# Performance work log

Hardware: AMD Instinct MI355X
Metric: run time of the kernel (lower is better)

The kernel has to match this reference:

```python
import jax, jax.numpy as jnp
import numpy as np

EPS_LN = 1e-5

def layer_norm(x, g, b):
    mu = x.mean(-1, keepdims=True)
    var = ((x - mu) ** 2).mean(-1, keepdims=True)
    return (x - mu) / jnp.sqrt(var + EPS_LN) * g + b

def spike(x):
    # MultiSpike: quantized spike activation, forward = clip(round(x), 0, 4)
    return jnp.clip(jnp.round(x), 0.0, 4.0)

def setup_inputs() -> dict:
    key = jax.random.key(0)
    ks = jax.random.split(key, 8)
    B, C, H, W = 16, 256, 56, 56
    hid = 128
    inp = {}
    inp['feature_map'] = jax.random.normal(ks[0], (B, C, H, W), jnp.float32)
    inp['audio_feature'] = jax.random.normal(ks[1], (B, 1, C), jnp.float32)
    # MINE params
    inp['w1'] = jax.random.normal(ks[2], (hid, 2 * C), jnp.float32) / np.sqrt(2 * C)
    inp['b1'] = jnp.zeros((hid,), jnp.float32)
    inp['g1'] = jnp.ones((hid,), jnp.float32)
    inp['beta1'] = jnp.zeros((hid,), jnp.float32)
    inp['w2'] = jax.random.normal(ks[3], (hid // 2, hid), jnp.float32) / np.sqrt(hid)
    inp['b2'] = jnp.zeros((hid // 2,), jnp.float32)
    inp['g2'] = jnp.ones((hid // 2,), jnp.float32)
    inp['beta2'] = jnp.zeros((hid // 2,), jnp.float32)
    inp['w3'] = jax.random.normal(ks[4], (1, hid // 2), jnp.float32) / np.sqrt(hid // 2)
    inp['b3'] = jnp.zeros((1,), jnp.float32)
    # MI params
    inp['pw'] = jax.random.normal(ks[5], (C, C), jnp.float32) / np.sqrt(C)
    inp['pb'] = jnp.zeros((C,), jnp.float32)
    inp['pg'] = jnp.ones((C,), jnp.float32)
    inp['pbeta'] = jnp.zeros((C,), jnp.float32)
    return inp

def reference(feature_map, audio_feature, w1, b1, g1, beta1, w2, b2, g2, beta2,
              w3, b3, pw, pb, pg, pbeta):
    B, C, H, W = feature_map.shape
    # visual tokens: [B*H*W, C]
    visual = feature_map.transpose(0, 2, 3, 1).reshape(B * H * W, C)
    # broadcast audio to every spatial position: [B*H*W, C]
    audio = jnp.broadcast_to(audio_feature[:, 0][:, None, None, :], (B, H, W, C)).reshape(B * H * W, C)
    # MINE MLP on joint features
    joint = jnp.concatenate([visual, audio], axis=1)            # [BHW, 2C]
    h = spike(layer_norm(joint @ w1.T + b1, g1, beta1))          # [BHW, 128]
    h = spike(layer_norm(h @ w2.T + b2, g2, beta2))              # [BHW, 64]
    mi = (h @ w3.T + b3)[:, 0]                                   # [BHW]
    mi_map = mi.reshape(B, 1, H * W)
    fm_flat = feature_map.reshape(B, C, H * W)
    # MI-weighted pooling: [B,1,C]
    x = jnp.einsum('bos,bcs->boc', mi_map, fm_flat)
    x = x @ pw.T + pb                                            # proj (dropout = eval identity)
    x = spike(layer_norm(x, pg, pbeta))                          # [B,1,C]
    fusion_map = jnp.einsum('bchw,bc->bchw', feature_map, x[:, 0])
    mi4 = mi_map.reshape(B, 1, H, W)
    mi4 = (mi4 - mi4.min()) / (mi4.max() - mi4.min() + 1e-6)     # global min-max norm
    return fusion_map, mi4
```

## Files before the change

kernel.cpp:

```cpp
#include <hip/hip_runtime.h>

#define HW 3136
#define NPOS 12845056
#define KC 32

__device__ __forceinline__ unsigned fkey(float f) {
  unsigned u = __float_as_uint(f);
  return (u & 0x80000000u) ? ~u : (u | 0x80000000u);
}
__device__ __forceinline__ float funkey(unsigned u) {
  return __uint_as_float((u & 0x80000000u) ? (u & 0x7FFFFFFFu) : ~u);
}
__device__ __forceinline__ float spikef(float x) {
  return fminf(fmaxf(rintf(x), 0.0f), 4.0f);
}

__global__ __launch_bounds__(256) void prep_kernel(
    const float* __restrict__ audio, const float* __restrict__ w1,
    const float* __restrict__ b1, const float* __restrict__ w2,
    float* __restrict__ a_pre, float* __restrict__ w1t,
    float* __restrict__ w2t, float* __restrict__ pool,
    unsigned* __restrict__ mm)
{
  __shared__ float au[256];
  const int bx = blockIdx.x, t = threadIdx.x;
  if (bx < 128) {
    int idx = bx * 256 + t;
    int c = idx >> 7, j = idx & 127;
    w1t[idx] = w1[j * 512 + c];
  } else if (bx < 160) {
    int idx = (bx - 128) * 256 + t;
    int k = idx >> 6, j2 = idx & 63;
    w2t[idx] = w2[j2 * 128 + k];
  } else if (bx < 176) {
    int b = bx - 160;
    au[t] = audio[b * 256 + t];
    __syncthreads();
    int w = t >> 6, l = t & 63;
    float a0 = au[l], a1 = au[l + 64], a2 = au[l + 128], a3 = au[l + 192];
    for (int jj = 0; jj < 32; ++jj) {
      int j = w * 32 + jj;
      const float* row = w1 + j * 512 + 256;
      float s = row[l] * a0 + row[l + 64] * a1 + row[l + 128] * a2 + row[l + 192] * a3;
      #pragma unroll
      for (int off = 32; off; off >>= 1) s += __shfl_xor(s, off);
      if (l == 0) a_pre[b * 128 + j] = s + b1[j];
    }
  } else {
    for (int i = t; i < 4096; i += 256) pool[i] = 0.0f;
    if (t == 0) { mm[0] = 0xFFFFFFFFu; mm[1] = 0u; }
  }
}

__global__ __launch_bounds__(256, 3) void mlp_kernel(
    const float* __restrict__ fm, const float* __restrict__ w1t,
    const float* __restrict__ w2t, const float* __restrict__ b2,
    const float* __restrict__ w3, const float* __restrict__ b3,
    const float* __restrict__ g1, const float* __restrict__ be1,
    const float* __restrict__ g2, const float* __restrict__ be2,
    const float* __restrict__ a_pre, float* __restrict__ mi_out,
    float* __restrict__ pool, unsigned* __restrict__ mm)
{
  __shared__ __align__(16) unsigned char smem[49152];
  __shared__ float red1[16][64];
  __shared__ float miL[64];

  float* fmb = (float*)smem;
  float* wb1 = (float*)(smem + 16384);
  float* h1f = (float*)smem;
  float* w2b = (float*)(smem + 32768);

  const int b  = blockIdx.y;
  const int s0 = blockIdx.x * 64;
  const int t  = threadIdx.x;
  const int l  = t & 63;
  const int w  = t >> 6;
  const int pg = t & 15;
  const int jg = t >> 4;

  const float* fmblk = fm + (size_t)b * 256 * HW + s0;

  auto stage1 = [&](int ch, int bd) {
    const int r0 = w * 8;
    #pragma unroll
    for (int q = 0; q < 2; ++q) {
      int row = r0 + q * 4 + (l >> 4);
      const float* g = fmblk + (size_t)(ch * KC + row) * HW + (l & 15) * 4;
      float* d = fmb + (bd * KC + r0 + q * 4) * 64;
      __builtin_amdgcn_global_load_lds(
          (const __attribute__((address_space(1))) void*)g,
          (__attribute__((address_space(3))) void*)d, 16, 0, 0);
    }
    #pragma unroll
    for (int q = 0; q < 4; ++q) {
      int row = r0 + q * 2 + (l >> 5);
      const float* g = w1t + (size_t)(ch * KC + row) * 128 + (l & 31) * 4;
      float* d = wb1 + (bd * KC + r0 + q * 2) * 128;
      __builtin_amdgcn_global_load_lds(
          (const __attribute__((address_space(1))) void*)g,
          (__attribute__((address_space(3))) void*)d, 16, 0, 0);
    }
  };
  auto stage2 = [&](int kc, int bd) {
    const int r0 = w * 8;
    #pragma unroll
    for (int q = 0; q < 2; ++q) {
      int row = r0 + q * 4 + (l >> 4);
      const float* g = w2t + (size_t)(kc * KC + row) * 64 + (l & 15) * 4;
      float* d = w2b + (bd * KC + r0 + q * 4) * 64;
      __builtin_amdgcn_global_load_lds(
          (const __attribute__((address_space(1))) void*)g,
          (__attribute__((address_space(3))) void*)d, 16, 0, 0);
    }
  };

  float acc[4][8];
  #pragma unroll
  for (int pp = 0; pp < 4; ++pp)
    #pragma unroll
    for (int jj = 0; jj < 8; ++jj) acc[pp][jj] = 0.f;

  stage1(0, 0);
  #pragma unroll 1
  for (int ch = 0; ch < 8; ++ch) {
    __syncthreads();
    if (ch < 7) stage1(ch + 1, (ch + 1) & 1);
    const float* fb = fmb + (ch & 1) * KC * 64;
    const float* wb = wb1 + (ch & 1) * KC * 128;
    #pragma unroll 4
    for (int k = 0; k < KC; ++k) {
      float4 xf = *(const float4*)(fb + k * 64 + pg * 4);
      float4 w0 = *(const float4*)(wb + k * 128 + jg * 8);
      float4 w1v = *(const float4*)(wb + k * 128 + jg * 8 + 4);
      float xs[4] = {xf.x, xf.y, xf.z, xf.w};
      float wv[8] = {w0.x, w0.y, w0.z, w0.w, w1v.x, w1v.y, w1v.z, w1v.w};
      #pragma unroll
      for (int pp = 0; pp < 4; ++pp)
        #pragma unroll
        for (int jj = 0; jj < 8; ++jj)
          acc[pp][jj] = fmaf(xs[pp], wv[jj], acc[pp][jj]);
    }
  }
  {
    float4 a0 = *(const float4*)(a_pre + b * 128 + jg * 8);
    float4 a1 = *(const float4*)(a_pre + b * 128 + jg * 8 + 4);
    float aw[8] = {a0.x, a0.y, a0.z, a0.w, a1.x, a1.y, a1.z, a1.w};
    #pragma unroll
    for (int pp = 0; pp < 4; ++pp)
      #pragma unroll
      for (int jj = 0; jj < 8; ++jj) acc[pp][jj] += aw[jj];
  }

  {
    float4 ps;
    float* p = &ps.x;
    #pragma unroll
    for (int pp = 0; pp < 4; ++pp) {
      float s = 0.f;
      #pragma unroll
      for (int jj = 0; jj < 8; ++jj) s += acc[pp][jj];
      p[pp] = s;
    }
    __syncthreads();
    *(float4*)&red1[jg][pg * 4] = ps;
  }
  __syncthreads();
  float mu[4];
  {
    float4 s = make_float4(0.f, 0.f, 0.f, 0.f);
    #pragma unroll
    for (int q = 0; q < 16; ++q) {
      float4 v = *(const float4*)&red1[q][pg * 4];
      s.x += v.x; s.y += v.y; s.z += v.z; s.w += v.w;
    }
    mu[0] = s.x * (1.0f/128.0f); mu[1] = s.y * (1.0f/128.0f);
    mu[2] = s.z * (1.0f/128.0f); mu[3] = s.w * (1.0f/128.0f);
  }
  __syncthreads();
  {
    float4 vs;
    float* p = &vs.x;
    #pragma unroll
    for (int pp = 0; pp < 4; ++pp) {
      float s = 0.f;
      #pragma unroll
      for (int jj = 0; jj < 8; ++jj) { float d = acc[pp][jj] - mu[pp]; s = fmaf(d, d, s); }
      p[pp] = s;
    }
    *(float4*)&red1[jg][pg * 4] = vs;
  }
  __syncthreads();
  float inv[4];
  {
    float4 s = make_float4(0.f, 0.f, 0.f, 0.f);
    #pragma unroll
    for (int q = 0; q < 16; ++q) {
      float4 v = *(const float4*)&red1[q][pg * 4];
      s.x += v.x; s.y += v.y; s.z += v.z; s.w += v.w;
    }
    inv[0] = 1.0f / sqrtf(s.x * (1.0f/128.0f) + 1e-5f);
    inv[1] = 1.0f / sqrtf(s.y * (1.0f/128.0f) + 1e-5f);
    inv[2] = 1.0f / sqrtf(s.z * (1.0f/128.0f) + 1e-5f);
    inv[3] = 1.0f / sqrtf(s.w * (1.0f/128.0f) + 1e-5f);
  }
  __syncthreads();

  stage2(0, 0);
  {
    float4 g1a = *(const float4*)(g1 + jg * 8);
    float4 g1b = *(const float4*)(g1 + jg * 8 + 4);
    float4 ba  = *(const float4*)(be1 + jg * 8);
    float4 bb  = *(const float4*)(be1 + jg * 8 + 4);
    float gv[8] = {g1a.x, g1a.y, g1a.z, g1a.w, g1b.x, g1b.y, g1b.z, g1b.w};
    float bv[8] = {ba.x, ba.y, ba.z, ba.w, bb.x, bb.y, bb.z, bb.w};
    #pragma unroll
    for (int jj = 0; jj < 8; ++jj) {
      float4 hv;
      hv.x = spikef((acc[0][jj] - mu[0]) * inv[0] * gv[jj] + bv[jj]);
      hv.y = spikef((acc[1][jj] - mu[1]) * inv[1] * gv[jj] + bv[jj]);
      hv.z = spikef((acc[2][jj] - mu[2]) * inv[2] * gv[jj] + bv[jj]);
      hv.w = spikef((acc[3][jj] - mu[3]) * inv[3] * gv[jj] + bv[jj]);
      *(float4*)(h1f + (jg * 8 + jj) * 64 + pg * 4) = hv;
    }
  }
  __syncthreads();

  float a2[4][4];
  #pragma unroll
  for (int pp = 0; pp < 4; ++pp)
    #pragma unroll
    for (int jj = 0; jj < 4; ++jj) a2[pp][jj] = 0.f;
  #pragma unroll 1
  for (int kc = 0; kc < 4; ++kc) {
    if (kc < 3) stage2(kc + 1, (kc + 1) & 1);
    const float* wb = w2b + (kc & 1) * KC * 64;
    #pragma unroll 4
    for (int k = 0; k < KC; ++k) {
      float4 hf = *(const float4*)(h1f + (kc * KC + k) * 64 + pg * 4);
      float4 wv4 = *(const float4*)(wb + k * 64 + jg * 4);
      float hs[4] = {hf.x, hf.y, hf.z, hf.w};
      float wv[4] = {wv4.x, wv4.y, wv4.z, wv4.w};
      #pragma unroll
      for (int pp = 0; pp < 4; ++pp)
        #pragma unroll
        for (int jj = 0; jj < 4; ++jj)
          a2[pp][jj] = fmaf(hs[pp], wv[jj], a2[pp][jj]);
    }
    __syncthreads();
  }

  float h2[4][4];
  {
    float4 b2v = *(const float4*)(b2 + jg * 4);
    float bb[4] = {b2v.x, b2v.y, b2v.z, b2v.w};
    float4 ps;
    float* p = &ps.x;
    #pragma unroll
    for (int pp = 0; pp < 4; ++pp) {
      float s = 0.f;
      #pragma unroll
      for (int jj = 0; jj < 4; ++jj) { h2[pp][jj] = a2[pp][jj] + bb[jj]; s += h2[pp][jj]; }
      p[pp] = s;
    }
    *(float4*)&red1[jg][pg * 4] = ps;
  }
  __syncthreads();
  float mu2[4];
  {
    float4 s = make_float4(0.f, 0.f, 0.f, 0.f);
    #pragma unroll
    for (int q = 0; q < 16; ++q) {
      float4 v = *(const float4*)&red1[q][pg * 4];
      s.x += v.x; s.y += v.y; s.z += v.z; s.w += v.w;
    }
    mu2[0] = s.x * (1.0f/64.0f); mu2[1] = s.y * (1.0f/64.0f);
    mu2[2] = s.z * (1.0f/64.0f); mu2[3] = s.w * (1.0f/64.0f);
  }
  __syncthreads();
  {
    float4 vs;
    float* p = &vs.x;
    #pragma unroll
    for (int pp = 0; pp < 4; ++pp) {
      float s = 0.f;
      #pragma unroll
      for (int jj = 0; jj < 4; ++jj) { float d = h2[pp][jj] - mu2[pp]; s = fmaf(d, d, s); }
      p[pp] = s;
    }
    *(float4*)&red1[jg][pg * 4] = vs;
  }
  __syncthreads();
  float inv2[4];
  {
    float4 s = make_float4(0.f, 0.f, 0.f, 0.f);
    #pragma unroll
    for (int q = 0; q < 16; ++q) {
      float4 v = *(const float4*)&red1[q][pg * 4];
      s.x += v.x; s.y += v.y; s.z += v.z; s.w += v.w;
    }
    inv2[0] = 1.0f / sqrtf(s.x * (1.0f/64.0f) + 1e-5f);
    inv2[1] = 1.0f / sqrtf(s.y * (1.0f/64.0f) + 1e-5f);
    inv2[2] = 1.0f / sqrtf(s.z * (1.0f/64.0f) + 1e-5f);
    inv2[3] = 1.0f / sqrtf(s.w * (1.0f/64.0f) + 1e-5f);
  }
  __syncthreads();
  {
    float4 g2v = *(const float4*)(g2 + jg * 4);
    float4 be2v = *(const float4*)(be2 + jg * 4);
    float4 w3v = *(const float4*)(w3 + jg * 4);
    float gv[4] = {g2v.x, g2v.y, g2v.z, g2v.w};
    float bv[4] = {be2v.x, be2v.y, be2v.z, be2v.w};
    float wv[4] = {w3v.x, w3v.y, w3v.z, w3v.w};
    float4 ps;
    float* p = &ps.x;
    #pragma unroll
    for (int pp = 0; pp < 4; ++pp) {
      float s = 0.f;
      #pragma unroll
      for (int jj = 0; jj < 4; ++jj) {
        float sp = spikef((h2[pp][jj] - mu2[pp]) * inv2[pp] * gv[jj] + bv[jj]);
        s = fmaf(sp, wv[jj], s);
      }
      p[pp] = s;
    }
    *(float4*)&red1[jg][pg * 4] = ps;
  }
  __syncthreads();
  if (t < 16) {
    float4 s = make_float4(0.f, 0.f, 0.f, 0.f);
    #pragma unroll
    for (int q = 0; q < 16; ++q) {
      float4 v = *(const float4*)&red1[q][pg * 4];
      s.x += v.x; s.y += v.y; s.z += v.z; s.w += v.w;
    }
    float b3v = b3[0];
    float4 miv = make_float4(s.x + b3v, s.y + b3v, s.z + b3v, s.w + b3v);
    *(float4*)(mi_out + b * HW + s0 + pg * 4) = miv;
    *(float4*)(miL + pg * 4) = miv;
    float mn = fminf(fminf(miv.x, miv.y), fminf(miv.z, miv.w));
    float mx = fmaxf(fmaxf(miv.x, miv.y), fmaxf(miv.z, miv.w));
    #pragma unroll
    for (int off = 8; off; off >>= 1) {
      mn = fminf(mn, __shfl_xor(mn, off));
      mx = fmaxf(mx, __shfl_xor(mx, off));
    }
    if (t == 0) {
      unsigned kmn = fkey(mn), kmx = fkey(mx);
      volatile unsigned* vmm = (volatile unsigned*)mm;
      if (kmn < vmm[0]) atomicMin(&mm[0], kmn);
      if (kmx > vmm[1]) atomicMax(&mm[1], kmx);
    }
  }
  __syncthreads();

  const float miv = miL[l];
  const float* fmp = fmblk + l;
  #pragma unroll 4
  for (int ci = 0; ci < 64; ++ci) {
    int c = (w << 6) + ci;
    float v = fmp[(size_t)c * HW] * miv;
    #pragma unroll
    for (int off = 32; off; off >>= 1) v += __shfl_xor(v, off);
    if (l == 0) atomicAdd(&pool[b * 256 + c], v);
  }
}

__global__ __launch_bounds__(256) void scale_kernel(
    const float* __restrict__ pool, const float* __restrict__ pw,
    const float* __restrict__ pb, const float* __restrict__ pg,
    const float* __restrict__ pbeta, float* __restrict__ scale,
    const unsigned* __restrict__ mm, float* __restrict__ gpar)
{
  __shared__ float pl[256];
  __shared__ float xsh[256];
  __shared__ float rs[4], rs2[4];
  int b = blockIdx.x, t = threadIdx.x;
  pl[t] = pool[b*256 + t];
  __syncthreads();
  int w = t >> 6, l = t & 63;
  float p0 = pl[l], p1 = pl[l+64], p2 = pl[l+128], p3 = pl[l+192];
  for (int jj = 0; jj < 64; ++jj) {
    int j = w*64 + jj;
    const float* row = pw + j*256;
    float s = row[l]*p0 + row[l+64]*p1 + row[l+128]*p2 + row[l+192]*p3;
    #pragma unroll
    for (int off = 32; off; off >>= 1) s += __shfl_xor(s, off);
    if (l == 0) xsh[j] = s;
  }
  __syncthreads();
  float x = xsh[t] + pb[t];
  float s = x;
  #pragma unroll
  for (int off = 32; off; off >>= 1) s += __shfl_xor(s, off);
  if (l == 0) rs[w] = s;
  __syncthreads();
  float mu = (rs[0]+rs[1]+rs[2]+rs[3]) * (1.0f/256.0f);
  float d = x - mu;
  float s2 = d*d;
  #pragma unroll
  for (int off = 32; off; off >>= 1) s2 += __shfl_xor(s2, off);
  if (l == 0) rs2[w] = s2;
  __syncthreads();
  float var = (rs2[0]+rs2[1]+rs2[2]+rs2[3]) * (1.0f/256.0f);
  float v = d / sqrtf(var + 1e-5f) * pg[t] + pbeta[t];
  scale[b*256 + t] = spikef(v);
  if (b == 0 && t == 0) {
    float mn = funkey(mm[0]), mx = funkey(mm[1]);
    gpar[0] = mn;
    gpar[1] = mx - mn + 1e-6f;
  }
}

__global__ __launch_bounds__(256) void fuse_kernel(
    const float4* __restrict__ fm4, const float* __restrict__ scale,
    const float4* __restrict__ mi4, const float* __restrict__ gpar,
    float4* __restrict__ out4, float4* __restrict__ mi4out)
{
  const int c = blockIdx.x, b = blockIdx.y, t = threadIdx.x;
  if (c < 256) {
    float s = scale[b * 256 + c];
    size_t base = ((size_t)b * 256 + c) * 784;
    #pragma unroll
    for (int i = 0; i < 3; ++i) {
      int idx = t + i * 256;
      float4 v = fm4[base + idx];
      out4[base + idx] = make_float4(v.x*s, v.y*s, v.z*s, v.w*s);
    }
    int idx = t + 768;
    if (idx < 784) {
      float4 v = fm4[base + idx];
      out4[base + idx] = make_float4(v.x*s, v.y*s, v.z*s, v.w*s);
    }
  } else {
    float gmin = gpar[0], den = gpar[1];
    size_t base = (size_t)b * 784;
    #pragma unroll
    for (int i = 0; i < 3; ++i) {
      int idx = t + i * 256;
      float4 v = mi4[base + idx];
      mi4out[base + idx] = make_float4((v.x-gmin)/den, (v.y-gmin)/den,
                                       (v.z-gmin)/den, (v.w-gmin)/den);
    }
    int idx = t + 768;
    if (idx < 784) {
      float4 v = mi4[base + idx];
      mi4out[base + idx] = make_float4((v.x-gmin)/den, (v.y-gmin)/den,
                                       (v.z-gmin)/den, (v.w-gmin)/den);
    }
  }
}

extern "C" void kernel_launch(void* const* d_in, const int* in_sizes, int n_in,
                              void* d_out, int out_size, void* d_ws, size_t ws_size,
                              hipStream_t stream)
{
  const float* fm    = (const float*)d_in[0];
  const float* audio = (const float*)d_in[1];
  const float* w1    = (const float*)d_in[2];
  const float* b1    = (const float*)d_in[3];
  const float* g1    = (const float*)d_in[4];
  const float* be1   = (const float*)d_in[5];
  const float* w2    = (const float*)d_in[6];
  const float* b2    = (const float*)d_in[7];
  const float* g2    = (const float*)d_in[8];
  const float* be2   = (const float*)d_in[9];
  const float* w3    = (const float*)d_in[10];
  const float* b3    = (const float*)d_in[11];
  const float* pw    = (const float*)d_in[12];
  const float* pb    = (const float*)d_in[13];
  const float* pg    = (const float*)d_in[14];
  const float* pbeta = (const float*)d_in[15];

  float* ws    = (float*)d_ws;
  float* a_pre = ws;
  float* pool  = ws + 2048;
  float* scale = ws + 6144;
  float* mi    = ws + 10240;
  float* w1t   = ws + 60416;
  float* w2t   = ws + 93184;
  unsigned* mm = (unsigned*)(ws + 101376);
  float* gpar  = ws + 101378;

  float* out    = (float*)d_out;
  float* mi4out = out + NPOS;

  prep_kernel<<<177, 256, 0, stream>>>(audio, w1, b1, w2, a_pre, w1t, w2t,
                                       pool, mm);
  mlp_kernel<<<dim3(49, 16), 256, 0, stream>>>(fm, w1t, w2t, b2, w3, b3,
                                               g1, be1, g2, be2,
                                               a_pre, mi, pool, mm);
  scale_kernel<<<16, 256, 0, stream>>>(pool, pw, pb, pg, pbeta, scale, mm, gpar);
  fuse_kernel<<<dim3(257, 16), 256, 0, stream>>>((const float4*)fm, scale,
                                                 (const float4*)mi, gpar,
                                                 (float4*)out, (float4*)mi4out);
}
```

Before: 308.3 us.

## Restructure MLP kernel to one position per lane with wave-uniform weight reads

Replaces the LDS-staged, double-buffered register-tiled GEMM in the MLP kernel with a mapping where each lane owns one spatial position and each wave owns a slice of output features. Weights are read directly from global memory at wave-uniform addresses, so they can be served as scalar or broadcast loads, and activations are read straight from the feature map. LayerNorm reductions become a simple 4-wave sum through a small shared array. This removes the LDS staging traffic and many barriers, but gives up the 4x8 register reuse of x across features and relies on cached global weight reads.

Result: faster. 287.0 us (-6.9%).

```diff
diff --git a/kernel.cpp b/kernel.cpp
--- a/kernel.cpp
+++ b/kernel.cpp
@@ -2,7 +2,6 @@
 
 #define HW 3136
 #define NPOS 12845056
-#define KC 32
 
 __device__ __forceinline__ unsigned fkey(float f) {
   unsigned u = __float_as_uint(f);
@@ -61,307 +60,162 @@
     const float* __restrict__ a_pre, float* __restrict__ mi_out,
     float* __restrict__ pool, unsigned* __restrict__ mm)
 {
-  __shared__ __align__(16) unsigned char smem[49152];
-  __shared__ float red1[16][64];
-  __shared__ float miL[64];
-
-  float* fmb = (float*)smem;
-  float* wb1 = (float*)(smem + 16384);
-  float* h1f = (float*)smem;
-  float* w2b = (float*)(smem + 32768);
+  __shared__ float h1f[128 * 64];
+  __shared__ float red[8][64];
 
   const int b  = blockIdx.y;
   const int s0 = blockIdx.x * 64;
   const int t  = threadIdx.x;
   const int l  = t & 63;
-  const int w  = t >> 6;
-  const int pg = t & 15;
-  const int jg = t >> 4;
+  const int wv = __builtin_amdgcn_readfirstlane(t >> 6);
 
   const float* fmblk = fm + (size_t)b * 256 * HW + s0;
 
-  auto stage1 = [&](int ch, int bd) {
-    const int r0 = w * 8;
-    #pragma unroll
-    for (int q = 0; q < 2; ++q) {
-      int row = r0 + q * 4 + (l >> 4);
-      const float* g = fmblk + (size_t)(ch * KC + row) * HW + (l & 15) * 4;
-      float* d = fmb + (bd * KC + r0 + q * 4) * 64;
-      __builtin_amdgcn_global_load_lds(
-          (const __attribute__((address_space(1))) void*)g,
-          (__attribute__((address_space(3))) void*)d, 16, 0, 0);
-    }
+  float acc[32];
+  #pragma unroll
+  for (int j = 0; j < 32; ++j) acc[j] = 0.f;
+  {
+    const float*  fp = fmblk + l;
+    const float4* wr = (const float4*)(w1t + wv * 32);
+    #pragma unroll 4
+    for (int k = 0; k < 256; ++k) {
+      float x = *fp; fp += HW;
+      #pragma unroll
+      for (int q = 0; q < 8; ++q) {
+        float4 w4 = wr[q];
+        acc[4*q+0] = fmaf(x, w4.x, acc[4*q+0]);
+        acc[4*q+1] = fmaf(x, w4.y, acc[4*q+1]);
+        acc[4*q+2] = fmaf(x, w4.z, acc[4*q+2]);
+        acc[4*q+3] = fmaf(x, w4.w, acc[4*q+3]);
+      }
+      wr += 32;
+    }
+  }
+  {
+    const float4* ap = (const float4*)(a_pre + b * 128 + wv * 32);
+    #pragma unroll
+    for (int q = 0; q < 8; ++q) {
+      float4 a4 = ap[q];
+      acc[4*q+0] += a4.x; acc[4*q+1] += a4.y;
+      acc[4*q+2] += a4.z; acc[4*q+3] += a4.w;
+    }
+  }
+
+  float mu, inv;
+  {
+    float s = 0.f;
+    #pragma unroll
+    for (int j = 0; j < 32; ++j) s += acc[j];
+    red[wv][l] = s;
+    __syncthreads();
+    mu = (red[0][l] + red[1][l] + red[2][l] + red[3][l]) * (1.0f/128.0f);
+    float s2 = 0.f;
+    #pragma unroll
+    for (int j = 0; j < 32; ++j) { float d = acc[j] - mu; s2 = fmaf(d, d, s2); }
+    red[4 + wv][l] = s2;
+    __syncthreads();
+    float var = (red[4][l] + red[5][l] + red[6][l] + red[7][l]) * (1.0f/128.0f);
+    inv = 1.0f / sqrtf(var + 1e-5f);
+  }
+
+  {
+    const float* gp = g1  + wv * 32;
+    const float* bp = be1 + wv * 32;
+    #pragma unroll
+    for (int j = 0; j < 32; ++j) {
+      float h = spikef((acc[j] - mu) * inv * gp[j] + bp[j]);
+      h1f[(wv * 32 + j) * 64 + l] = h;
+    }
+  }
+  __syncthreads();
+
+  float a2[16];
+  #pragma unroll
+  for (int j = 0; j < 16; ++j) a2[j] = 0.f;
+  {
+    const float*  hp = h1f + l;
+    const float4* wr = (const float4*)(w2t + wv * 16);
+    #pragma unroll 4
+    for (int k = 0; k < 128; ++k) {
+      float h = *hp; hp += 64;
+      #pragma unroll
+      for (int q = 0; q < 4; ++q) {
+        float4 w4 = wr[q];
+        a2[4*q+0] = fmaf(h, w4.x, a2[4*q+0]);
+        a2[4*q+1] = fmaf(h, w4.y, a2[4*q+1]);
+        a2[4*q+2] = fmaf(h, w4.z, a2[4*q+2]);
+        a2[4*q+3] = fmaf(h, w4.w, a2[4*q+3]);
+      }
+      wr += 16;
+    }
+  }
+  {
+    const float4* bp = (const float4*)(b2 + wv * 16);
     #pragma unroll
     for (int q = 0; q < 4; ++q) {
-      int row = r0 + q * 2 + (l >> 5);
-      const float* g = w1t + (size_t)(ch * KC + row) * 128 + (l & 31) * 4;
-      float* d = wb1 + (bd * KC + r0 + q * 2) * 128;
-      __builtin_amdgcn_global_load_lds(
-          (const __attribute__((address_space(1))) void*)g,
-          (__attribute__((address_space(3))) void*)d, 16, 0, 0);
-    }
-  };
-  auto stage2 = [&](int kc, int bd) {
-    const int r0 = w * 8;
-    #pragma unroll
-    for (int q = 0; q < 2; ++q) {
-      int row = r0 + q * 4 + (l >> 4);
-      const float* g = w2t + (size_t)(kc * KC + row) * 64 + (l & 15) * 4;
-      float* d = w2b + (bd * KC + r0 + q * 4) * 64;
-      __builtin_amdgcn_global_load_lds(
-          (const __attribute__((address_space(1))) void*)g,
-          (__attribute__((address_space(3))) void*)d, 16, 0, 0);
-    }
-  };
-
-  float acc[4][8];
-  #pragma unroll
-  for (int pp = 0; pp < 4; ++pp)
-    #pragma unroll
-    for (int jj = 0; jj < 8; ++jj) acc[pp][jj] = 0.f;
-
-  stage1(0, 0);
-  #pragma unroll 1
-  for (int ch = 0; ch < 8; ++ch) {
-    __syncthreads();
-    if (ch < 7) stage1(ch + 1, (ch + 1) & 1);
-    const float* fb = fmb + (ch & 1) * KC * 64;
-    const float* wb = wb1 + (ch & 1) * KC * 128;
-    #pragma unroll 4
-    for (int k = 0; k < KC; ++k) {
-      float4 xf = *(const float4*)(fb + k * 64 + pg * 4);
-      float4 w0 = *(const float4*)(wb + k * 128 + jg * 8);
-      float4 w1v = *(const float4*)(wb + k * 128 + jg * 8 + 4);
-      float xs[4] = {xf.x, xf.y, xf.z, xf.w};
-      float wv[8] = {w0.x, w0.y, w0.z, w0.w, w1v.x, w1v.y, w1v.z, w1v.w};
-      #pragma unroll
-      for (int pp = 0; pp < 4; ++pp)
-        #pragma unroll
-        for (int jj = 0; jj < 8; ++jj)
-          acc[pp][jj] = fmaf(xs[pp], wv[jj], acc[pp][jj]);
-    }
-  }
-  {
-    float4 a0 = *(const float4*)(a_pre + b * 128 + jg * 8);
-    float4 a1 = *(const float4*)(a_pre + b * 128 + jg * 8 + 4);
-    float aw[8] = {a0.x, a0.y, a0.z, a0.w, a1.x, a1.y, a1.z, a1.w};
-    #pragma unroll
-    for (int pp = 0; pp < 4; ++pp)
-      #pragma unroll
-      for (int jj = 0; jj < 8; ++jj) acc[pp][jj] += aw[jj];
-  }
-
-  {
-    float4 ps;
-    float* p = &ps.x;
-    #pragma unroll
-    for (int pp = 0; pp < 4; ++pp) {
-      float s = 0.f;
-      #pragma unroll
-      for (int jj = 0; jj < 8; ++jj) s += acc[pp][jj];
-      p[pp] = s;
-    }
-    __syncthreads();
-    *(float4*)&red1[jg][pg * 4] = ps;
-  }
-  __syncthreads();
-  float mu[4];
-  {
-    float4 s = make_float4(0.f, 0.f, 0.f, 0.f);
-    #pragma unroll
-    for (int q = 0; q < 16; ++q) {
-      float4 v = *(const float4*)&red1[q][pg * 4];
-      s.x += v.x; s.y += v.y; s.z += v.z; s.w += v.w;
-    }
-    mu[0] = s.x * (1.0f/128.0f); mu[1] = s.y * (1.0f/128.0f);
-    mu[2] = s.z * (1.0f/128.0f); mu[3] = s.w * (1.0f/128.0f);
-  }
-  __syncthreads();
-  {
-    float4 vs;
-    float* p = &vs.x;
-    #pragma unroll
-    for (int pp = 0; pp < 4; ++pp) {
-      float s = 0.f;
-      #pragma unroll
-      for (int jj = 0; jj < 8; ++jj) { float d = acc[pp][jj] - mu[pp]; s = fmaf(d, d, s); }
-      p[pp] = s;
-    }
-    *(float4*)&red1[jg][pg * 4] = vs;
-  }
-  __syncthreads();
-  float inv[4];
-  {
-    float4 s = make_float4(0.f, 0.f, 0.f, 0.f);
-    #pragma unroll
-    for (int q = 0; q < 16; ++q) {
-      float4 v = *(const float4*)&red1[q][pg * 4];
-      s.x += v.x; s.y += v.y; s.z += v.z; s.w += v.w;
-    }
-    inv[0] = 1.0f / sqrtf(s.x * (1.0f/128.0f) + 1e-5f);
-    inv[1] = 1.0f / sqrtf(s.y * (1.0f/128.0f) + 1e-5f);
-    inv[2] = 1.0f / sqrtf(s.z * (1.0f/128.0f) + 1e-5f);
-    inv[3] = 1.0f / sqrtf(s.w * (1.0f/128.0f) + 1e-5f);
-  }
-  __syncthreads();
-
-  stage2(0, 0);
-  {
-    float4 g1a = *(const float4*)(g1 + jg * 8);
-    float4 g1b = *(const float4*)(g1 + jg * 8 + 4);
-    float4 ba  = *(const float4*)(be1 + jg * 8);
-    float4 bb  = *(const float4*)(be1 + jg * 8 + 4);
-    float gv[8] = {g1a.x, g1a.y, g1a.z, g1a.w, g1b.x, g1b.y, g1b.z, g1b.w};
-    float bv[8] = {ba.x, ba.y, ba.z, ba.w, bb.x, bb.y, bb.z, bb.w};
-    #pragma unroll
-    for (int jj = 0; jj < 8; ++jj) {
-      float4 hv;
-      hv.x = spikef((acc[0][jj] - mu[0]) * inv[0] * gv[jj] + bv[jj]);
-      hv.y = spikef((acc[1][jj] - mu[1]) * inv[1] * gv[jj] + bv[jj]);
-      hv.z = spikef((acc[2][jj] - mu[2]) * inv[2] * gv[jj] + bv[jj]);
-      hv.w = spikef((acc[3][jj] - mu[3]) * inv[3] * gv[jj] + bv[jj]);
-      *(float4*)(h1f + (jg * 8 + jj) * 64 + pg * 4) = hv;
-    }
-  }
-  __syncthreads();
-
-  float a2[4][4];
-  #pragma unroll
-  for (int pp = 0; pp < 4; ++pp)
-    #pragma unroll
-    for (int jj = 0; jj < 4; ++jj) a2[pp][jj] = 0.f;
-  #pragma unroll 1
-  for (int kc = 0; kc < 4; ++kc) {
-    if (kc < 3) stage2(kc + 1, (kc + 1) & 1);
-    const float* wb = w2b + (kc & 1) * KC * 64;
-    #pragma unroll 4
-    for (int k = 0; k < KC; ++k) {
-      float4 hf = *(const float4*)(h1f + (kc * KC + k) * 64 + pg * 4);
-      float4 wv4 = *(const float4*)(wb + k * 64 + jg * 4);
-      float hs[4] = {hf.x, hf.y, hf.z, hf.w};
-      float wv[4] = {wv4.x, wv4.y, wv4.z, wv4.w};
-      #pragma unroll
-      for (int pp = 0; pp < 4; ++pp)
-        #pragma unroll
-        for (int jj = 0; jj < 4; ++jj)
-          a2[pp][jj] = fmaf(hs[pp], wv[jj], a2[pp][jj]);
-    }
-    __syncthreads();
-  }
-
-  float h2[4][4];
-  {
-    float4 b2v = *(const float4*)(b2 + jg * 4);
-    float bb[4] = {b2v.x, b2v.y, b2v.z, b2v.w};
-    float4 ps;
-    float* p = &ps.x;
-    #pragma unroll
-    for (int pp = 0; pp < 4; ++pp) {
-      float s = 0.f;
-      #pragma unroll
-      for (int jj = 0; jj < 4; ++jj) { h2[pp][jj] = a2[pp][jj] + bb[jj]; s += h2[pp][jj]; }
-      p[pp] = s;
-    }
-    *(float4*)&red1[jg][pg * 4] = ps;
-  }
-  __syncthreads();
-  float mu2[4];
-  {
-    float4 s = make_float4(0.f, 0.f, 0.f, 0.f);
-    #pragma unroll
-    for (int q = 0; q < 16; ++q) {
-      float4 v = *(const float4*)&red1[q][pg * 4];
-      s.x += v.x; s.y += v.y; s.z += v.z; s.w += v.w;
-    }
-    mu2[0] = s.x * (1.0f/64.0f); mu2[1] = s.y * (1.0f/64.0f);
-    mu2[2] = s.z * (1.0f/64.0f); mu2[3] = s.w * (1.0f/64.0f);
-  }
-  __syncthreads();
-  {
-    float4 vs;
-    float* p = &vs.x;
-    #pragma unroll
-    for (int pp = 0; pp < 4; ++pp) {
-      float s = 0.f;
-      #pragma unroll
-      for (int jj = 0; jj < 4; ++jj) { float d = h2[pp][jj] - mu2[pp]; s = fmaf(d, d, s); }
-      p[pp] = s;
-    }
-    *(float4*)&red1[jg][pg * 4] = vs;
-  }
-  __syncthreads();
-  float inv2[4];
-  {
-    float4 s = make_float4(0.f, 0.f, 0.f, 0.f);
-    #pragma unroll
-    for (int q = 0; q < 16; ++q) {
-      float4 v = *(const float4*)&red1[q][pg * 4];
-      s.x += v.x; s.y += v.y; s.z += v.z; s.w += v.w;
-    }
-    inv2[0] = 1.0f / sqrtf(s.x * (1.0f/64.0f) + 1e-5f);
-    inv2[1] = 1.0f / sqrtf(s.y * (1.0f/64.0f) + 1e-5f);
-    inv2[2] = 1.0f / sqrtf(s.z * (1.0f/64.0f) + 1e-5f);
-    inv2[3] = 1.0f / sqrtf(s.w * (1.0f/64.0f) + 1e-5f);
-  }
-  __syncthreads();
-  {
-    float4 g2v = *(const float4*)(g2 + jg * 4);
-    float4 be2v = *(const float4*)(be2 + jg * 4);
-    float4 w3v = *(const float4*)(w3 + jg * 4);
-    float gv[4] = {g2v.x, g2v.y, g2v.z, g2v.w};
-    float bv[4] = {be2v.x, be2v.y, be2v.z, be2v.w};
-    float wv[4] = {w3v.x, w3v.y, w3v.z, w3v.w};
-    float4 ps;
-    float* p = &ps.x;
-    #pragma unroll
-    for (int pp = 0; pp < 4; ++pp) {
-      float s = 0.f;
-      #pragma unroll
-      for (int jj = 0; jj < 4; ++jj) {
-        float sp = spikef((h2[pp][jj] - mu2[pp]) * inv2[pp] * gv[jj] + bv[jj]);
-        s = fmaf(sp, wv[jj], s);
-      }
-      p[pp] = s;
-    }
-    *(float4*)&red1[jg][pg * 4] = ps;
-  }
-  __syncthreads();
-  if (t < 16) {
-    float4 s = make_float4(0.f, 0.f, 0.f, 0.f);
-    #pragma unroll
-    for (int q = 0; q < 16; ++q) {
-      float4 v = *(const float4*)&red1[q][pg * 4];
-      s.x += v.x; s.y += v.y; s.z += v.z; s.w += v.w;
-    }
-    float b3v = b3[0];
-    float4 miv = make_float4(s.x + b3v, s.y + b3v, s.z + b3v, s.w + b3v);
-    *(float4*)(mi_out + b * HW + s0 + pg * 4) = miv;
-    *(float4*)(miL + pg * 4) = miv;
-    float mn = fminf(fminf(miv.x, miv.y), fminf(miv.z, miv.w));
-    float mx = fmaxf(fmaxf(miv.x, miv.y), fmaxf(miv.z, miv.w));
-    #pragma unroll
-    for (int off = 8; off; off >>= 1) {
+      float4 b4 = bp[q];
+      a2[4*q+0] += b4.x; a2[4*q+1] += b4.y;
+      a2[4*q+2] += b4.z; a2[4*q+3] += b4.w;
+    }
+  }
+
+  float mu2, inv2;
+  {
+    float s = 0.f;
+    #pragma unroll
+    for (int j = 0; j < 16; ++j) s += a2[j];
+    red[wv][l] = s;
+    __syncthreads();
+    mu2 = (red[0][l] + red[1][l] + red[2][l] + red[3][l]) * (1.0f/64.0f);
+    float s2 = 0.f;
+    #pragma unroll
+    for (int j = 0; j < 16; ++j) { float d = a2[j] - mu2; s2 = fmaf(d, d, s2); }
+    red[4 + wv][l] = s2;
+    __syncthreads();
+    float var = (red[4][l] + red[5][l] + red[6][l] + red[7][l]) * (1.0f/64.0f);
+    inv2 = 1.0f / sqrtf(var + 1e-5f);
+  }
+
+  {
+    const float* gp = g2  + wv * 16;
+    const float* bp = be2 + wv * 16;
+    const float* wp = w3  + wv * 16;
+    float p = 0.f;
+    #pragma unroll
+    for (int j = 0; j < 16; ++j) {
+      float sp = spikef((a2[j] - mu2) * inv2 * gp[j] + bp[j]);
+      p = fmaf(sp, wp[j], p);
+    }
+    red[wv][l] = p;
+  }
+  __syncthreads();
+  const float mi = red[0][l] + red[1][l] + red[2][l] + red[3][l] + b3[0];
+
+  if (wv == 0) {
+    mi_out[b * HW + s0 + l] = mi;
+    float mn = mi, mx = mi;
+    #pragma unroll
+    for (int off = 32; off; off >>= 1) {
       mn = fminf(mn, __shfl_xor(mn, off));
       mx = fmaxf(mx, __shfl_xor(mx, off));
     }
-    if (t == 0) {
+    if (l == 0) {
       unsigned kmn = fkey(mn), kmx = fkey(mx);
       volatile unsigned* vmm = (volatile unsigned*)mm;
       if (kmn < vmm[0]) atomicMin(&mm[0], kmn);
       if (kmx > vmm[1]) atomicMax(&mm[1], kmx);
     }
   }
-  __syncthreads();
-
-  const float miv = miL[l];
-  const float* fmp = fmblk + l;
-  #pragma unroll 4
-  for (int ci = 0; ci < 64; ++ci) {
-    int c = (w << 6) + ci;
-    float v = fmp[(size_t)c * HW] * miv;
-    #pragma unroll
-    for (int off = 32; off; off >>= 1) v += __shfl_xor(v, off);
-    if (l == 0) atomicAdd(&pool[b * 256 + c], v);
+
+  {
+    const float* fp = fmblk + l + (size_t)(wv << 6) * HW;
+    #pragma unroll 4
+    for (int ci = 0; ci < 64; ++ci) {
+      float v = *fp * mi; fp += HW;
+      #pragma unroll
+      for (int off = 32; off; off >>= 1) v += __shfl_xor(v, off);
+      if (l == 0) atomicAdd(&pool[b * 256 + (wv << 6) + ci], v);
+    }
   }
 }
 
```
